# Kernel optimization log

Hardware: AMD Instinct MI355X
Metric: run time of the kernel (lower is better)

## Reference

```python
import jax, jax.numpy as jnp
import numpy as np

E = 800_000
D = 64
N_NODES = 50_000


def setup_inputs() -> dict:
    key = jax.random.key(0)
    k1, k2, k3 = jax.random.split(key, 3)
    M = jax.random.normal(k1, (E, D), dtype=jnp.float32)
    edge_index = jax.random.randint(k2, (2, E), 0, N_NODES, dtype=jnp.int64)
    rev_index = jax.random.randint(k3, (E,), 0, E, dtype=jnp.int64)
    return {"M": M, "edge_index": edge_index, "rev_index": rev_index, "dim_size": N_NODES}


def reference(M, edge_index, rev_index, dim_size):
    # directed=True sum-aggregation variant of Aggregation.forward
    src, dest = edge_index[0], edge_index[1]
    # gather: scatter-add edge messages into destination nodes -> [dim_size, D]
    M_v = jax.ops.segment_sum(M, dest, num_segments=dim_size)
    # edge-wise gather by src node, minus reverse-edge message
    return M_v[src] - M[rev_index]
```

## Files before the change

kernel.cpp:

```cpp
#include <hip/hip_runtime.h>


#define D 64
#define N_NODES 50000
#define SCAN_THREADS 1024

__global__ void agg_hist(const int* __restrict__ dest, int* __restrict__ counts, int E) {
    int e = blockIdx.x * blockDim.x + threadIdx.x;
    if (e < E) atomicAdd(counts + dest[e], 1);
}

__global__ void agg_scan(int* __restrict__ data) {
    __shared__ int sums[SCAN_THREADS];
    const int N = N_NODES;
    int t = threadIdx.x;
    const int chunk = (N + SCAN_THREADS - 1) / SCAN_THREADS;
    int start = t * chunk;
    int end   = min(start + chunk, N);
    int s = 0;
    for (int i = start; i < end; ++i) s += data[i];
    sums[t] = s;
    __syncthreads();
    for (int off = 1; off < SCAN_THREADS; off <<= 1) {
        int v = sums[t];
        int u = (t >= off) ? sums[t - off] : 0;
        __syncthreads();
        sums[t] = v + u;
        __syncthreads();
    }
    int run = (t == 0) ? 0 : sums[t - 1];
    for (int i = start; i < end; ++i) {
        int c = data[i];
        data[i] = run;
        run += c;
    }
    if (t == SCAN_THREADS - 1) data[N] = run;
}

__global__ void agg_bin(const int* __restrict__ dest, int* __restrict__ cursor,
                        int* __restrict__ order, int E) {
    int e = blockIdx.x * blockDim.x + threadIdx.x;
    if (e < E) {
        int pos = atomicAdd(cursor + dest[e], 1);
        order[pos] = e;
    }
}

__global__ void agg_reduce(const float* __restrict__ M,
                           const int* __restrict__ order,
                           const int* __restrict__ offsets,
                           float* __restrict__ Mv) {
    int lane = threadIdx.x & 63;
    int node = (blockIdx.x * blockDim.x + threadIdx.x) >> 6;
    if (node >= N_NODES) return;
    int beg = offsets[node];
    int end = offsets[node + 1];
    float acc = 0.f;
    int i = beg;
    for (; i + 4 <= end; i += 4) {
        int e0 = order[i];
        int e1 = order[i + 1];
        int e2 = order[i + 2];
        int e3 = order[i + 3];
        float a0 = M[(size_t)e0 * D + lane];
        float a1 = M[(size_t)e1 * D + lane];
        float a2 = M[(size_t)e2 * D + lane];
        float a3 = M[(size_t)e3 * D + lane];
        acc += (a0 + a1) + (a2 + a3);
    }
    for (; i < end; ++i) acc += M[(size_t)order[i] * D + lane];
    Mv[(size_t)node * D + lane] = acc;
}

__global__ void agg_gather(const float* __restrict__ Mv,
                           const float* __restrict__ M,
                           const int* __restrict__ src,
                           const int* __restrict__ rev,
                           float* __restrict__ out,
                           int E) {
    int gid = blockIdx.x * blockDim.x + threadIdx.x;
    int e  = gid >> 4;
    int c4 = gid & 15;
    if (e >= E) return;
    int s = src[e];
    int r = rev[e];
    float4 a = reinterpret_cast<const float4*>(Mv + (size_t)s * D)[c4];
    float4 b = reinterpret_cast<const float4*>(M  + (size_t)r * D)[c4];
    float4 o;
    o.x = a.x - b.x;
    o.y = a.y - b.y;
    o.z = a.z - b.z;
    o.w = a.w - b.w;
    reinterpret_cast<float4*>(out + (size_t)e * D)[c4] = o;
}

extern "C" void kernel_launch(void* const* d_in, const int* in_sizes, int n_in,
                              void* d_out, int out_size, void* d_ws, size_t ws_size,
                              hipStream_t stream) {
    const float* M   = (const float*)d_in[0];
    const int*   ei  = (const int*)d_in[1];
    const int*   rev = (const int*)d_in[2];

    int E = in_sizes[0] / D;
    const int* src  = ei;
    const int* dest = ei + E;

    int*   offsets = (int*)d_ws;
    int*   cursor  = offsets + 50304;
    int*   order   = cursor + 50304;
    float* Mv      = (float*)(order + 800128);

    hipMemsetAsync(offsets, 0, (N_NODES + 1) * sizeof(int), stream);

    int eb = (E + 255) / 256;
    agg_hist<<<eb, 256, 0, stream>>>(dest, offsets, E);
    agg_scan<<<1, SCAN_THREADS, 0, stream>>>(offsets);
    hipMemcpyAsync(cursor, offsets, (N_NODES + 1) * sizeof(int),
                   hipMemcpyDeviceToDevice, stream);
    agg_bin<<<eb, 256, 0, stream>>>(dest, cursor, order, E);

    int rb = (N_NODES * 64 + 255) / 256;
    agg_reduce<<<rb, 256, 0, stream>>>(M, order, offsets, Mv);

    int gb = (E * 16 + 255) / 256;
    agg_gather<<<gb, 256, 0, stream>>>(Mv, M, src, rev, (float*)d_out, E);
}
```

Measured before the change: 581.5 us.

## Replace sort-based segment sum with direct float atomic scatter-add

Drops the histogram, scan, binning and CSR reduce pipeline and instead scatter-adds each edge's message row into a zeroed node buffer with hardware float atomics (unsafeAtomicAdd). This removes several launches, the single-block serial scan and the index-indirect reduce, in exchange for 51.2M float atomics contending on 50k rows. The gather kernel now writes its output with nontemporal stores. Atomic accumulation makes the summation order nondeterministic.

```diff
diff --git a/kernel.cpp b/kernel.cpp
--- a/kernel.cpp
+++ b/kernel.cpp
@@ -3,73 +3,23 @@
 
 #define D 64
 #define N_NODES 50000
-#define SCAN_THREADS 1024
 
-__global__ void agg_hist(const int* __restrict__ dest, int* __restrict__ counts, int E) {
-    int e = blockIdx.x * blockDim.x + threadIdx.x;
-    if (e < E) atomicAdd(counts + dest[e], 1);
-}
+typedef float f4 __attribute__((ext_vector_type(4)));
 
-__global__ void agg_scan(int* __restrict__ data) {
-    __shared__ int sums[SCAN_THREADS];
-    const int N = N_NODES;
-    int t = threadIdx.x;
-    const int chunk = (N + SCAN_THREADS - 1) / SCAN_THREADS;
-    int start = t * chunk;
-    int end   = min(start + chunk, N);
-    int s = 0;
-    for (int i = start; i < end; ++i) s += data[i];
-    sums[t] = s;
-    __syncthreads();
-    for (int off = 1; off < SCAN_THREADS; off <<= 1) {
-        int v = sums[t];
-        int u = (t >= off) ? sums[t - off] : 0;
-        __syncthreads();
-        sums[t] = v + u;
-        __syncthreads();
-    }
-    int run = (t == 0) ? 0 : sums[t - 1];
-    for (int i = start; i < end; ++i) {
-        int c = data[i];
-        data[i] = run;
-        run += c;
-    }
-    if (t == SCAN_THREADS - 1) data[N] = run;
-}
-
-__global__ void agg_bin(const int* __restrict__ dest, int* __restrict__ cursor,
-                        int* __restrict__ order, int E) {
-    int e = blockIdx.x * blockDim.x + threadIdx.x;
-    if (e < E) {
-        int pos = atomicAdd(cursor + dest[e], 1);
-        order[pos] = e;
-    }
-}
-
-__global__ void agg_reduce(const float* __restrict__ M,
-                           const int* __restrict__ order,
-                           const int* __restrict__ offsets,
-                           float* __restrict__ Mv) {
-    int lane = threadIdx.x & 63;
-    int node = (blockIdx.x * blockDim.x + threadIdx.x) >> 6;
-    if (node >= N_NODES) return;
-    int beg = offsets[node];
-    int end = offsets[node + 1];
-    float acc = 0.f;
-    int i = beg;
-    for (; i + 4 <= end; i += 4) {
-        int e0 = order[i];
-        int e1 = order[i + 1];
-        int e2 = order[i + 2];
-        int e3 = order[i + 3];
-        float a0 = M[(size_t)e0 * D + lane];
-        float a1 = M[(size_t)e1 * D + lane];
-        float a2 = M[(size_t)e2 * D + lane];
-        float a3 = M[(size_t)e3 * D + lane];
-        acc += (a0 + a1) + (a2 + a3);
-    }
-    for (; i < end; ++i) acc += M[(size_t)order[i] * D + lane];
-    Mv[(size_t)node * D + lane] = acc;
+__global__ void agg_atomic(const float* __restrict__ M,
+                           const int* __restrict__ dest,
+                           float* __restrict__ Mv, int E) {
+    int gid = blockIdx.x * blockDim.x + threadIdx.x;
+    int e  = gid >> 4;
+    int c4 = gid & 15;
+    if (e >= E) return;
+    f4 v = reinterpret_cast<const f4*>(M + (size_t)e * D)[c4];
+    int d = dest[e];
+    float* p = Mv + (size_t)d * D + c4 * 4;
+    unsafeAtomicAdd(p + 0, v.x);
+    unsafeAtomicAdd(p + 1, v.y);
+    unsafeAtomicAdd(p + 2, v.z);
+    unsafeAtomicAdd(p + 3, v.w);
 }
 
 __global__ void agg_gather(const float* __restrict__ Mv,
@@ -84,14 +34,10 @@
     if (e >= E) return;
     int s = src[e];
     int r = rev[e];
-    float4 a = reinterpret_cast<const float4*>(Mv + (size_t)s * D)[c4];
-    float4 b = reinterpret_cast<const float4*>(M  + (size_t)r * D)[c4];
-    float4 o;
-    o.x = a.x - b.x;
-    o.y = a.y - b.y;
-    o.z = a.z - b.z;
-    o.w = a.w - b.w;
-    reinterpret_cast<float4*>(out + (size_t)e * D)[c4] = o;
+    f4 a = reinterpret_cast<const f4*>(Mv + (size_t)s * D)[c4];
+    f4 b = reinterpret_cast<const f4*>(M  + (size_t)r * D)[c4];
+    f4 o = a - b;
+    __builtin_nontemporal_store(o, reinterpret_cast<f4*>(out + (size_t)e * D) + c4);
 }
 
 extern "C" void kernel_launch(void* const* d_in, const int* in_sizes, int n_in,
@@ -105,23 +51,13 @@
     const int* src  = ei;
     const int* dest = ei + E;
 
-    int*   offsets = (int*)d_ws;
-    int*   cursor  = offsets + 50304;
-    int*   order   = cursor + 50304;
-    float* Mv      = (float*)(order + 800128);
+    float* Mv = (float*)d_ws;
 
-    hipMemsetAsync(offsets, 0, (N_NODES + 1) * sizeof(int), stream);
+    hipMemsetAsync(Mv, 0, (size_t)N_NODES * D * sizeof(float), stream);
 
-    int eb = (E + 255) / 256;
-    agg_hist<<<eb, 256, 0, stream>>>(dest, offsets, E);
-    agg_scan<<<1, SCAN_THREADS, 0, stream>>>(offsets);
-    hipMemcpyAsync(cursor, offsets, (N_NODES + 1) * sizeof(int),
-                   hipMemcpyDeviceToDevice, stream);
-    agg_bin<<<eb, 256, 0, stream>>>(dest, cursor, order, E);
+    int ab = (int)(((size_t)E * 16 + 255) / 256);
+    agg_atomic<<<ab, 256, 0, stream>>>(M, dest, Mv, E);
 
-    int rb = (N_NODES * 64 + 255) / 256;
-    agg_reduce<<<rb, 256, 0, stream>>>(M, order, offsets, Mv);
-
-    int gb = (E * 16 + 255) / 256;
+    int gb = (int)(((size_t)E * 16 + 255) / 256);
     agg_gather<<<gb, 256, 0, stream>>>(Mv, M, src, rev, (float*)d_out, E);
 }
```

Measured after the change: 1.003 ms. 72.5% more time.
